# Kernel optimization log

Measured on AMD Instinct MI355X. Metric: run time of the kernel, lower is better.

## Reference

```python
import jax, jax.numpy as jnp
import numpy as np

EPS = 1e-12  # torch F.normalize eps
RBF_SCALE = 10.0


def _l2norm(x, axis=-1):
    n = jnp.sqrt(jnp.sum(x * x, axis=axis, keepdims=True))
    return x / jnp.maximum(n, EPS)


def setup_inputs() -> dict:
    key = jax.random.key(0)
    k1, k2, k3 = jax.random.split(key, 3)
    N, D, C = 32768, 1024, 2048
    inp = jax.random.normal(k1, (N, D), dtype=jnp.float32)
    pos = jax.random.normal(k2, (C, D), dtype=jnp.float32)
    # offset is initialized to zeros in torch; use small random values so the
    # output is non-trivial for kernel correctness testing.
    offset = 0.01 * jax.random.normal(k3, (C, D), dtype=jnp.float32)
    return {"inp": inp, "pos": pos, "offset": offset}


def reference(inp, pos, offset):
    a = _l2norm(inp)                       # [N, D]
    b = _l2norm(pos)                       # [C, D]
    dist = 1.0 - jnp.einsum('nd,cd->nc', a, b)   # [N, C] cosine distance
    w = jnp.exp(-RBF_SCALE * dist)               # RBF cluster weights
    # The torch for-loop  out += offset[i] * dist[:, i, None]  is a GEMM:
    out = inp + jnp.einsum('nc,cd->nd', w, offset)
    out = _l2norm(out)
    offset_reg = jnp.sum(offset * offset)
    return (out, offset_reg)
```

## Files before the change

### kernel.cpp

```cpp
#include <hip/hip_runtime.h>

typedef float  f32x4  __attribute__((ext_vector_type(4)));
typedef float  f32x16 __attribute__((ext_vector_type(16)));
typedef int    i32x4  __attribute__((ext_vector_type(4)));
typedef int    i32x8  __attribute__((ext_vector_type(8)));

#define AS1 __attribute__((address_space(1)))
#define AS3 __attribute__((address_space(3)))

__device__ __forceinline__ unsigned int f2e4m3(float x){
    union{float f; unsigned u;} v; v.f = x;
    unsigned s = (v.u >> 24) & 0x80u;
    float ax = fabsf(x);
    if (ax > 448.0f) ax = 448.0f;
    if (ax < 0.015625f){
        int d = (int)__builtin_rintf(ax * 512.0f);
        return s | (unsigned)d;
    }
    v.f = ax;
    unsigned u = v.u + 0x7ffffu + ((v.u >> 20) & 1u);
    unsigned E = (u >> 23) - 120u;
    unsigned M = (u >> 20) & 7u;
    return s | (E << 3) | M;
}

__device__ __forceinline__ unsigned int pk4_e4m3(float x0, float x1, float x2, float x3){
    return f2e4m3(x0) | (f2e4m3(x1) << 8) | (f2e4m3(x2) << 16) | (f2e4m3(x3) << 24);
}

__device__ __forceinline__ void gload16(const unsigned char* g, const char* l){
    __builtin_amdgcn_global_load_lds((const AS1 void*)g, (AS3 void*)l, 16, 0, 0);
}

__device__ __forceinline__ i32x8 ld_frag(const char* p0, const char* p1){
    i32x4 lo = *(const i32x4*)p0;
    i32x4 hi = *(const i32x4*)p1;
    return __builtin_shufflevector(lo, hi, 0,1,2,3,4,5,6,7);
}

#define GBAR() do{ asm volatile("" ::: "memory"); __builtin_amdgcn_s_barrier(); \
                   asm volatile("" ::: "memory"); }while(0)
#define VMW(N)  asm volatile("s_waitcnt vmcnt(" #N ")" ::: "memory")
#define LGKM0() asm volatile("s_waitcnt lgkmcnt(0)" ::: "memory")

__global__ __launch_bounds__(256) void norm_rows_fp8(const float* __restrict__ in,
                                                     unsigned int* __restrict__ out){
    const int row = blockIdx.x;
    const int t   = threadIdx.x;
    f32x4 x = ((const f32x4*)(in + (size_t)row * 1024))[t];
    float ss = x[0]*x[0] + x[1]*x[1] + x[2]*x[2] + x[3]*x[3];
    #pragma unroll
    for (int o = 32; o > 0; o >>= 1) ss += __shfl_xor(ss, o);
    __shared__ float red[4];
    if ((t & 63) == 0) red[t >> 6] = ss;
    __syncthreads();
    float tot = red[0] + red[1] + red[2] + red[3];
    float inv = 16.0f / fmaxf(sqrtf(tot), 1e-12f);
    out[(size_t)row * 256 + t] = pk4_e4m3(x[0]*inv, x[1]*inv, x[2]*inv, x[3]*inv);
}

__global__ __launch_bounds__(256) void norm_rows_f32(float* __restrict__ buf){
    const int row = blockIdx.x;
    const int t   = threadIdx.x;
    f32x4* p = (f32x4*)(buf + (size_t)row * 1024);
    f32x4 x = p[t];
    float ss = x[0]*x[0] + x[1]*x[1] + x[2]*x[2] + x[3]*x[3];
    #pragma unroll
    for (int o = 32; o > 0; o >>= 1) ss += __shfl_xor(ss, o);
    __shared__ float red[4];
    if ((t & 63) == 0) red[t >> 6] = ss;
    __syncthreads();
    float tot = red[0] + red[1] + red[2] + red[3];
    float inv = 1.0f / fmaxf(sqrtf(tot), 1e-12f);
    p[t] = x * inv;
}

__global__ __launch_bounds__(256) void transpose_off(const float* __restrict__ off,
                                                     unsigned char* __restrict__ offt,
                                                     float* __restrict__ reg_out){
    __shared__ unsigned char t_lds[64][68];
    const int t  = threadIdx.x;
    const int c0 = blockIdx.x * 64;
    const int d0 = blockIdx.y * 64;
    float ss = 0.f;
    #pragma unroll
    for (int p = 0; p < 4; ++p){
        int c  = p * 16 + (t >> 4);
        int dq = t & 15;
        f32x4 v = *(const f32x4*)(off + (size_t)(c0 + c) * 1024 + d0 + dq * 4);
        ss += v[0]*v[0] + v[1]*v[1] + v[2]*v[2] + v[3]*v[3];
        #pragma unroll
        for (int j = 0; j < 4; ++j) t_lds[dq * 4 + j][c] = (unsigned char)f2e4m3(v[j] * 64.0f);
    }
    __syncthreads();
    #pragma unroll
    for (int p = 0; p < 4; ++p){
        int d  = p * 16 + (t >> 4);
        int cq = t & 15;
        unsigned int o = *(const unsigned int*)&t_lds[d][cq * 4];
        *(unsigned int*)(offt + (size_t)(d0 + d) * 2048 + c0 + cq * 4) = o;
    }
    #pragma unroll
    for (int o = 32; o > 0; o >>= 1) ss += __shfl_xor(ss, o);
    __shared__ float red[4];
    if ((t & 63) == 0) red[t >> 6] = ss;
    __syncthreads();
    if (t == 0) atomicAdd(reg_out, red[0] + red[1] + red[2] + red[3]);
}

template<int EPI, int SA, int SB>
__global__ __launch_bounds__(512, 2)
void gemm256(const unsigned char* __restrict__ A, int lda,
             const unsigned char* __restrict__ B, int ldb,
             int K,
             unsigned char* __restrict__ Wout, int ldw,
             const float* __restrict__ Cadd, float* __restrict__ Fout, int ldo)
{
    extern __shared__ char smem[];
    const int tid  = threadIdx.x;

    int bx = blockIdx.x, by = blockIdx.y;
    {
        const int gx = gridDim.x, gy = gridDim.y;
        const int nwg = gx * gy;
        if ((nwg & 7) == 0){
            const int lid = bx + gx * by;
            const int q   = nwg >> 3;
            const int n   = (lid & 7) * q + (lid >> 3);
            const int sh  = 31 - __clz(gy);
            bx = n >> sh;
            by = n & (gy - 1);
        }
    }
    const int m0   = bx * 256;
    const int n0   = by * 256;
    const int wid  = tid >> 6, lane = tid & 63;
    const int wr   = wid >> 2, wc = wid & 3;
    const int l31  = lane & 31, hg = lane >> 5;

    const int srow = tid >> 2;
    const int sg   = (tid & 3) ^ ((tid >> 3) & 3);
    const unsigned char* sA0 = A + (size_t)(m0 + srow)       * lda + sg * 16;
    const unsigned char* sA1 = A + (size_t)(m0 + 128 + srow) * lda + sg * 16;
    const unsigned char* sB0 = B + (size_t)(n0 + srow)       * ldb + sg * 16;
    const unsigned char* sB1 = B + (size_t)(n0 + 128 + srow) * ldb + sg * 16;
    const int lp0 = tid * 16, lp1 = 8192 + tid * 16;

    auto stageA = [&](char* wb, int qbase, int koff){
        gload16(sA0 + koff, wb + qbase + lp0);
        gload16(sA1 + koff, wb + qbase + lp1);
    };
    auto stageB = [&](char* wb, int qbase, int koff){
        gload16(sB0 + koff, wb + qbase + lp0);
        gload16(sB1 + koff, wb + qbase + lp1);
    };

    int aoff[4][2], boff[2][2];
    #pragma unroll
    for (int m = 0; m < 4; ++m){
        int row = wr * 128 + m * 32 + l31;
        int sw  = (row >> 1) & 3;
        aoff[m][0] = row * 64 + (((hg << 1) | 0) ^ sw) * 16;
        aoff[m][1] = row * 64 + (((hg << 1) | 1) ^ sw) * 16;
    }
    #pragma unroll
    for (int n = 0; n < 2; ++n){
        int row = wc * 64 + n * 32 + l31;
        int sw  = (row >> 1) & 3;
        boff[n][0] = 16384 + row * 64 + (((hg << 1) | 0) ^ sw) * 16;
        boff[n][1] = 16384 + row * 64 + (((hg << 1) | 1) ^ sw) * 16;
    }

    f32x16 acc[4][2] = {};
    const int nsteps = K >> 7;

    {
        char* wb = smem;
        stageA(wb, 0,     0);  stageB(wb, 16384, 0);
        stageA(wb, 32768, 64); stageB(wb, 49152, 64);
    }
    VMW(4);
    GBAR();

#define RD_A2(dst, rbq, mb) { \
    dst[0] = ld_frag((rbq) + aoff[(mb)][0],   (rbq) + aoff[(mb)][1]); \
    dst[1] = ld_frag((rbq) + aoff[(mb)+1][0], (rbq) + aoff[(mb)+1][1]); }
#define RD_B2(dst, rbq) { \
    dst[0] = ld_frag((rbq) + boff[0][0], (rbq) + boff[0][1]); \
    dst[1] = ld_frag((rbq) + boff[1][0], (rbq) + boff[1][1]); }
#define MFMA4(mb, av, bv) { __builtin_amdgcn_s_setprio(1); \
    _Pragma("unroll") for (int mi = 0; mi < 2; ++mi) \
    _Pragma("unroll") for (int ni = 0; ni < 2; ++ni) \
        acc[(mb)+mi][ni] = __builtin_amdgcn_mfma_scale_f32_32x32x64_f8f6f4( \
            av[mi], bv[ni], acc[(mb)+mi][ni], 0, 0, 0, SA, 0, SB); \
    __builtin_amdgcn_s_setprio(0); }

    i32x8 fa[2], fb[2];

    #pragma unroll 1
    for (int t = 0; t < nsteps - 1; ++t){
        const char* rb = smem + (t & 1) * 65536;
        char*       wb = smem + ((t + 1) & 1) * 65536;
        const int   ke = (t + 1) * 128;
        RD_A2(fa, rb, 0); RD_B2(fb, rb);
        GBAR();
        stageA(wb, 0, ke);
        LGKM0();
        MFMA4(0, fa, fb);
        RD_A2(fa, rb, 2);
        VMW(2);
        GBAR();
        stageB(wb, 16384, ke);
        LGKM0();
        MFMA4(2, fa, fb);
        RD_A2(fa, rb + 32768, 0); RD_B2(fb, rb + 32768);
        GBAR();
        stageA(wb, 32768, ke + 64);
        LGKM0();
        MFMA4(0, fa, fb);
        RD_A2(fa, rb + 32768, 2);
        VMW(2);
        GBAR();
        stageB(wb, 49152, ke + 64);
        LGKM0();
        MFMA4(2, fa, fb);
    }
    {
        const char* rb = smem + ((nsteps - 1) & 1) * 65536;
        RD_A2(fa, rb, 0); RD_B2(fb, rb);
        GBAR();
        LGKM0();
        MFMA4(0, fa, fb);
        RD_A2(fa, rb, 2);
        VMW(0);
        GBAR();
        LGKM0();
        MFMA4(2, fa, fb);
        RD_A2(fa, rb + 32768, 0); RD_B2(fb, rb + 32768);
        GBAR();
        LGKM0();
        MFMA4(0, fa, fb);
        RD_A2(fa, rb + 32768, 2);
        GBAR();
        LGKM0();
        MFMA4(2, fa, fb);
    }
#undef RD_A2
#undef RD_B2
#undef MFMA4

    asm volatile("s_nop 7\n\ts_nop 7");

    #pragma unroll
    for (int m = 0; m < 4; ++m){
        #pragma unroll
        for (int n = 0; n < 2; ++n){
            const int grb = m0 + wr * 128 + m * 32;
            const int gc  = n0 + wc * 64  + n * 32 + l31;
            #pragma unroll
            for (int r = 0; r < 16; ++r){
                const int row = (r & 3) + 8 * (r >> 2) + 4 * hg;
                if (EPI == 1){
                    float w = __expf(10.0f * acc[m][n][r] - 10.0f) * 1024.0f;
                    Wout[(size_t)(grb + row) * ldw + gc] = (unsigned char)f2e4m3(w);
                } else {
                    Fout[(size_t)(grb + row) * ldo + gc] =
                        Cadd[(size_t)(grb + row) * ldo + gc] + acc[m][n][r];
                }
            }
        }
    }
}

extern "C" void kernel_launch(void* const* d_in, const int* in_sizes, int n_in,
                              void* d_out, int out_size, void* d_ws, size_t ws_size,
                              hipStream_t stream)
{
    (void)n_in; (void)out_size;
    const float* inp = (const float*)d_in[0];
    const float* pos = (const float*)d_in[1];
    const float* off = (const float*)d_in[2];
    float* out = (float*)d_out;

    const int D = 1024, C = 2048;
    const int N = in_sizes[0] / D;

    unsigned char* b_fp8 = (unsigned char*)d_ws;
    unsigned char* offt  = b_fp8 + (size_t)C * D;
    unsigned char* a_fp8 = offt + (size_t)D * C;
    size_t fixed = (size_t)C * D * 2;
    size_t avail = ws_size > fixed ? ws_size - fixed : 0;
    int Mc = 256;
    for (int cand = N; cand >= 256; cand >>= 1){
        if ((size_t)cand * (size_t)(D + C) <= avail){ Mc = cand; break; }
    }
    if (Mc > N) Mc = N;
    unsigned char* w_buf = a_fp8 + (size_t)Mc * D;

    hipFuncSetAttribute(reinterpret_cast<const void*>(&gemm256<1,123,123>),
                        hipFuncAttributeMaxDynamicSharedMemorySize, 131072);
    hipFuncSetAttribute(reinterpret_cast<const void*>(&gemm256<2,117,121>),
                        hipFuncAttributeMaxDynamicSharedMemorySize, 131072);

    float* reg_out = out + (size_t)N * D;
    hipMemsetAsync(reg_out, 0, sizeof(float), stream);

    transpose_off<<<dim3(C / 64, D / 64), 256, 0, stream>>>(off, offt, reg_out);
    norm_rows_fp8<<<C, 256, 0, stream>>>(pos, (unsigned int*)b_fp8);

    for (int r0 = 0; r0 < N; r0 += Mc){
        norm_rows_fp8<<<Mc, 256, 0, stream>>>(inp + (size_t)r0 * D, (unsigned int*)a_fp8);
        gemm256<1,123,123><<<dim3(Mc / 256, C / 256), 512, 131072, stream>>>(
            a_fp8, D, b_fp8, D, D, w_buf, C, nullptr, nullptr, 0);
        gemm256<2,117,121><<<dim3(Mc / 256, D / 256), 512, 131072, stream>>>(
            w_buf, C, offt, C, C, nullptr, 0, inp + (size_t)r0 * D, out + (size_t)r0 * D, D);
    }
    norm_rows_f32<<<N, 256, 0, stream>>>(out);
}
```

Measured before the change: 297.8 us.

## Shrink GEMM tile to 256x128 with triple-buffered LDS pipeline and hardware fp8 conversion

```diff
diff --git a/kernel.cpp b/kernel.cpp
--- a/kernel.cpp
+++ b/kernel.cpp
@@ -24,8 +24,14 @@
     return s | (E << 3) | M;
 }
 
-__device__ __forceinline__ unsigned int pk4_e4m3(float x0, float x1, float x2, float x3){
+__device__ __forceinline__ unsigned int pk4(float x0, float x1, float x2, float x3){
+#if __has_builtin(__builtin_amdgcn_cvt_pk_fp8_f32)
+    int u = __builtin_amdgcn_cvt_pk_fp8_f32(x0, x1, 0, false);
+    u     = __builtin_amdgcn_cvt_pk_fp8_f32(x2, x3, u, true);
+    return (unsigned)u;
+#else
     return f2e4m3(x0) | (f2e4m3(x1) << 8) | (f2e4m3(x2) << 16) | (f2e4m3(x3) << 24);
+#endif
 }
 
 __device__ __forceinline__ void gload16(const unsigned char* g, const char* l){
@@ -41,7 +47,6 @@
 #define GBAR() do{ asm volatile("" ::: "memory"); __builtin_amdgcn_s_barrier(); \
                    asm volatile("" ::: "memory"); }while(0)
 #define VMW(N)  asm volatile("s_waitcnt vmcnt(" #N ")" ::: "memory")
-#define LGKM0() asm volatile("s_waitcnt lgkmcnt(0)" ::: "memory")
 
 __global__ __launch_bounds__(256) void norm_rows_fp8(const float* __restrict__ in,
                                                      unsigned int* __restrict__ out){
@@ -56,7 +61,7 @@
     __syncthreads();
     float tot = red[0] + red[1] + red[2] + red[3];
     float inv = 16.0f / fmaxf(sqrtf(tot), 1e-12f);
-    out[(size_t)row * 256 + t] = pk4_e4m3(x[0]*inv, x[1]*inv, x[2]*inv, x[3]*inv);
+    out[(size_t)row * 256 + t] = pk4(x[0]*inv, x[1]*inv, x[2]*inv, x[3]*inv);
 }
 
 __global__ __launch_bounds__(256) void norm_rows_f32(float* __restrict__ buf){
@@ -89,8 +94,9 @@
         int dq = t & 15;
         f32x4 v = *(const f32x4*)(off + (size_t)(c0 + c) * 1024 + d0 + dq * 4);
         ss += v[0]*v[0] + v[1]*v[1] + v[2]*v[2] + v[3]*v[3];
+        unsigned u = pk4(v[0]*64.0f, v[1]*64.0f, v[2]*64.0f, v[3]*64.0f);
         #pragma unroll
-        for (int j = 0; j < 4; ++j) t_lds[dq * 4 + j][c] = (unsigned char)f2e4m3(v[j] * 64.0f);
+        for (int j = 0; j < 4; ++j) t_lds[dq * 4 + j][c] = (unsigned char)(u >> (8*j));
     }
     __syncthreads();
     #pragma unroll
@@ -109,7 +115,7 @@
 }
 
 template<int EPI, int SA, int SB>
-__global__ __launch_bounds__(512, 2)
+__global__ __launch_bounds__(256, 2)
 void gemm256(const unsigned char* __restrict__ A, int lda,
              const unsigned char* __restrict__ B, int ldb,
              int K,
@@ -133,26 +139,26 @@
         }
     }
     const int m0   = bx * 256;
-    const int n0   = by * 256;
+    const int n0   = by * 128;
     const int wid  = tid >> 6, lane = tid & 63;
-    const int wr   = wid >> 2, wc = wid & 3;
+    const int wr   = wid >> 1, wc = wid & 1;
     const int l31  = lane & 31, hg = lane >> 5;
 
     const int srow = tid >> 2;
     const int sg   = (tid & 3) ^ ((tid >> 3) & 3);
-    const unsigned char* sA0 = A + (size_t)(m0 + srow)       * lda + sg * 16;
-    const unsigned char* sA1 = A + (size_t)(m0 + 128 + srow) * lda + sg * 16;
-    const unsigned char* sB0 = B + (size_t)(n0 + srow)       * ldb + sg * 16;
-    const unsigned char* sB1 = B + (size_t)(n0 + 128 + srow) * ldb + sg * 16;
-    const int lp0 = tid * 16, lp1 = 8192 + tid * 16;
-
-    auto stageA = [&](char* wb, int qbase, int koff){
-        gload16(sA0 + koff, wb + qbase + lp0);
-        gload16(sA1 + koff, wb + qbase + lp1);
+    const unsigned char* sA = A + (size_t)(m0 + srow) * lda + sg * 16;
+    const unsigned char* sB = B + (size_t)(n0 + srow) * ldb + sg * 16;
+    const int lp = tid * 16;
+
+    auto stgA = [&](char* wb, int ke){
+        #pragma unroll
+        for (int j = 0; j < 4; ++j)
+            gload16(sA + (size_t)j * 64 * lda + ke, wb + j * 4096 + lp);
     };
-    auto stageB = [&](char* wb, int qbase, int koff){
-        gload16(sB0 + koff, wb + qbase + lp0);
-        gload16(sB1 + koff, wb + qbase + lp1);
+    auto stgB = [&](char* wb, int ke){
+        #pragma unroll
+        for (int j = 0; j < 2; ++j)
+            gload16(sB + (size_t)j * 64 * ldb + ke, wb + 16384 + j * 4096 + lp);
     };
 
     int aoff[4][2], boff[2][2];
@@ -172,81 +178,59 @@
     }
 
     f32x16 acc[4][2] = {};
-    const int nsteps = K >> 7;
-
-    {
-        char* wb = smem;
-        stageA(wb, 0,     0);  stageB(wb, 16384, 0);
-        stageA(wb, 32768, 64); stageB(wb, 49152, 64);
-    }
-    VMW(4);
-    GBAR();
-
-#define RD_A2(dst, rbq, mb) { \
-    dst[0] = ld_frag((rbq) + aoff[(mb)][0],   (rbq) + aoff[(mb)][1]); \
-    dst[1] = ld_frag((rbq) + aoff[(mb)+1][0], (rbq) + aoff[(mb)+1][1]); }
-#define RD_B2(dst, rbq) { \
-    dst[0] = ld_frag((rbq) + boff[0][0], (rbq) + boff[0][1]); \
-    dst[1] = ld_frag((rbq) + boff[1][0], (rbq) + boff[1][1]); }
-#define MFMA4(mb, av, bv) { __builtin_amdgcn_s_setprio(1); \
+    const int nsteps = K >> 6;
+
+#define RD_A(mb) { \
+    fa[0] = ld_frag(b0 + aoff[(mb)][0],   b0 + aoff[(mb)][1]); \
+    fa[1] = ld_frag(b0 + aoff[(mb)+1][0], b0 + aoff[(mb)+1][1]); }
+#define RD_B()   { \
+    fb[0] = ld_frag(b0 + boff[0][0], b0 + boff[0][1]); \
+    fb[1] = ld_frag(b0 + boff[1][0], b0 + boff[1][1]); }
+#define MFMA4(mb) { __builtin_amdgcn_s_setprio(1); \
     _Pragma("unroll") for (int mi = 0; mi < 2; ++mi) \
     _Pragma("unroll") for (int ni = 0; ni < 2; ++ni) \
         acc[(mb)+mi][ni] = __builtin_amdgcn_mfma_scale_f32_32x32x64_f8f6f4( \
-            av[mi], bv[ni], acc[(mb)+mi][ni], 0, 0, 0, SA, 0, SB); \
+            fa[mi], fb[ni], acc[(mb)+mi][ni], 0, 0, 0, SA, 0, SB); \
     __builtin_amdgcn_s_setprio(0); }
 
     i32x8 fa[2], fb[2];
-
+    char* b0 = smem;
+    char* b1 = smem + 24576;
+    char* b2 = smem + 49152;
+
+    stgA(b0, 0);  stgB(b0, 0);
+    stgA(b1, 64); stgB(b1, 64);
+    VMW(6);
+    GBAR();
+
+    int ke = 128;
     #pragma unroll 1
-    for (int t = 0; t < nsteps - 1; ++t){
-        const char* rb = smem + (t & 1) * 65536;
-        char*       wb = smem + ((t + 1) & 1) * 65536;
-        const int   ke = (t + 1) * 128;
-        RD_A2(fa, rb, 0); RD_B2(fb, rb);
+    for (int t = 0; t < nsteps - 2; ++t){
+        RD_A(0); RD_B();
+        stgA(b2, ke);
+        MFMA4(0);
+        RD_A(2);
+        stgB(b2, ke);
+        MFMA4(2);
+        VMW(6);
         GBAR();
-        stageA(wb, 0, ke);
-        LGKM0();
-        MFMA4(0, fa, fb);
-        RD_A2(fa, rb, 2);
-        VMW(2);
-        GBAR();
-        stageB(wb, 16384, ke);
-        LGKM0();
-        MFMA4(2, fa, fb);
-        RD_A2(fa, rb + 32768, 0); RD_B2(fb, rb + 32768);
-        GBAR();
-        stageA(wb, 32768, ke + 64);
-        LGKM0();
-        MFMA4(0, fa, fb);
-        RD_A2(fa, rb + 32768, 2);
-        VMW(2);
-        GBAR();
-        stageB(wb, 49152, ke + 64);
-        LGKM0();
-        MFMA4(2, fa, fb);
-    }
-    {
-        const char* rb = smem + ((nsteps - 1) & 1) * 65536;
-        RD_A2(fa, rb, 0); RD_B2(fb, rb);
-        GBAR();
-        LGKM0();
-        MFMA4(0, fa, fb);
-        RD_A2(fa, rb, 2);
-        VMW(0);
-        GBAR();
-        LGKM0();
-        MFMA4(2, fa, fb);
-        RD_A2(fa, rb + 32768, 0); RD_B2(fb, rb + 32768);
-        GBAR();
-        LGKM0();
-        MFMA4(0, fa, fb);
-        RD_A2(fa, rb + 32768, 2);
-        GBAR();
-        LGKM0();
-        MFMA4(2, fa, fb);
-    }
-#undef RD_A2
-#undef RD_B2
+        char* tmp = b0; b0 = b1; b1 = b2; b2 = tmp;
+        ke += 64;
+    }
+    RD_A(0); RD_B();
+    MFMA4(0);
+    RD_A(2);
+    MFMA4(2);
+    VMW(0);
+    GBAR();
+    { char* tmp = b0; b0 = b1; b1 = tmp; }
+    RD_A(0); RD_B();
+    MFMA4(0);
+    RD_A(2);
+    MFMA4(2);
+
+#undef RD_A
+#undef RD_B
 #undef MFMA4
 
     asm volatile("s_nop 7\n\ts_nop 7");
@@ -257,13 +241,25 @@
         for (int n = 0; n < 2; ++n){
             const int grb = m0 + wr * 128 + m * 32;
             const int gc  = n0 + wc * 64  + n * 32 + l31;
-            #pragma unroll
-            for (int r = 0; r < 16; ++r){
-                const int row = (r & 3) + 8 * (r >> 2) + 4 * hg;
-                if (EPI == 1){
-                    float w = __expf(10.0f * acc[m][n][r] - 10.0f) * 1024.0f;
-                    Wout[(size_t)(grb + row) * ldw + gc] = (unsigned char)f2e4m3(w);
-                } else {
+            if (EPI == 1){
+                #pragma unroll
+                for (int q = 0; q < 4; ++q){
+                    const int row0 = grb + 8 * q + 4 * hg;
+                    float w0 = exp2f(fmaf(14.4269504f, acc[m][n][4*q+0], -4.4269504f));
+                    float w1 = exp2f(fmaf(14.4269504f, acc[m][n][4*q+1], -4.4269504f));
+                    float w2 = exp2f(fmaf(14.4269504f, acc[m][n][4*q+2], -4.4269504f));
+                    float w3 = exp2f(fmaf(14.4269504f, acc[m][n][4*q+3], -4.4269504f));
+                    unsigned u = pk4(w0, w1, w2, w3);
+                    unsigned char* p = Wout + (size_t)row0 * ldw + gc;
+                    p[0]                = (unsigned char)u;
+                    p[(size_t)ldw]      = (unsigned char)(u >> 8);
+                    p[(size_t)ldw * 2]  = (unsigned char)(u >> 16);
+                    p[(size_t)ldw * 3]  = (unsigned char)(u >> 24);
+                }
+            } else {
+                #pragma unroll
+                for (int r = 0; r < 16; ++r){
+                    const int row = (r & 3) + 8 * (r >> 2) + 4 * hg;
                     Fout[(size_t)(grb + row) * ldo + gc] =
                         Cadd[(size_t)(grb + row) * ldo + gc] + acc[m][n][r];
                 }
@@ -298,9 +294,9 @@
     unsigned char* w_buf = a_fp8 + (size_t)Mc * D;
 
     hipFuncSetAttribute(reinterpret_cast<const void*>(&gemm256<1,123,123>),
-                        hipFuncAttributeMaxDynamicSharedMemorySize, 131072);
+                        hipFuncAttributeMaxDynamicSharedMemorySize, 73728);
     hipFuncSetAttribute(reinterpret_cast<const void*>(&gemm256<2,117,121>),
-                        hipFuncAttributeMaxDynamicSharedMemorySize, 131072);
+                        hipFuncAttributeMaxDynamicSharedMemorySize, 73728);
 
     float* reg_out = out + (size_t)N * D;
     hipMemsetAsync(reg_out, 0, sizeof(float), stream);
@@ -310,9 +306,9 @@
 
     for (int r0 = 0; r0 < N; r0 += Mc){
         norm_rows_fp8<<<Mc, 256, 0, stream>>>(inp + (size_t)r0 * D, (unsigned int*)a_fp8);
-        gemm256<1,123,123><<<dim3(Mc / 256, C / 256), 512, 131072, stream>>>(
+        gemm256<1,123,123><<<dim3(Mc / 256, C / 128), 256, 73728, stream>>>(
             a_fp8, D, b_fp8, D, D, w_buf, C, nullptr, nullptr, 0);
-        gemm256<2,117,121><<<dim3(Mc / 256, D / 256), 512, 131072, stream>>>(
+        gemm256<2,117,121><<<dim3(Mc / 256, D / 128), 256, 73728, stream>>>(
             w_buf, C, offt, C, C, nullptr, 0, inp + (size_t)r0 * D, out + (size_t)r0 * D, D);
     }
     norm_rows_f32<<<N, 256, 0, stream>>>(out);
```

Measured after the change: 279.0 us (median of 2 runs). 1.07x faster.
